# Performance work log

Hardware: AMD Instinct MI355X
Metric: run time of the kernel (lower is better)

The kernel has to match this reference:

```python
import jax, jax.numpy as jnp
import numpy as np
import math

D_MODEL = 1024
NUM_HEADS = 16
D_HEAD = D_MODEL // NUM_HEADS


def setup_inputs() -> dict:
    key = jax.random.key(0)
    ks = jax.random.split(key, 12)
    b, s = 2, 2048
    lim = 1.0 / math.sqrt(D_MODEL)
    def lin_w(k):
        return jax.random.uniform(k, (D_MODEL, D_MODEL), jnp.float32, -lim, lim)
    def lin_b(k):
        return jax.random.uniform(k, (D_MODEL,), jnp.float32, -lim, lim)
    return {
        "q": jax.random.normal(ks[0], (b, s, D_MODEL), jnp.float32),
        "k": jax.random.normal(ks[1], (b, s, D_MODEL), jnp.float32),
        "v": jax.random.normal(ks[2], (b, s, D_MODEL), jnp.float32),
        "mask": jax.random.randint(ks[3], (b, s, s), 0, 2, jnp.int32),
        "Wq": lin_w(ks[4]), "bq": lin_b(ks[5]),
        "Wk": lin_w(ks[6]), "bk": lin_b(ks[7]),
        "Wv": lin_w(ks[8]), "bv": lin_b(ks[9]),
        "Wo": lin_w(ks[10]), "bo": lin_b(ks[11]),
    }


def reference(q, k, v, mask, Wq, bq, Wk, bk, Wv, bv, Wo, bo):
    b, s, _ = q.shape
    h, dh = NUM_HEADS, D_HEAD
    # projections (torch Linear: x @ W.T + b), split heads -> (b, h, s, dh)
    qh = (q @ Wq.T + bq).reshape(b, s, h, dh).transpose(0, 2, 1, 3)
    kh = (k @ Wk.T + bk).reshape(b, s, h, dh).transpose(0, 2, 1, 3)
    vh = (v @ Wv.T + bv).reshape(b, s, h, dh).transpose(0, 2, 1, 3)
    # scaled dot-product scores (b, h, s_q, s_kv)
    scores = jnp.einsum("bhqd,bhkd->bhqk", qh, kh) / math.sqrt(dh)
    scores = jnp.where(mask[:, None, :, :] == 0, jnp.float32(-1e9), scores)
    score = jax.nn.softmax(scores, axis=-1)
    attn = jnp.einsum("bhqk,bhkd->bhqd", score, vh)  # (b, h, s, dh)
    # faithful to the torch code: raw reshape of (b, h, s, dh) -> (b, s, d_model)
    # WITHOUT transposing heads back (replicates the original's .view)
    out = attn.reshape(b, -1, D_MODEL) @ Wo.T + bo
    return out, score
```

## Files before the change

kernel.cpp:

```cpp
#include <hip/hip_runtime.h>

typedef __bf16 bf16_t;
typedef __bf16 bf16x4 __attribute__((ext_vector_type(4)));
typedef __bf16 bf16x8 __attribute__((ext_vector_type(8)));
typedef float f32x4 __attribute__((ext_vector_type(4)));

__device__ __forceinline__ void load_lds16(const void* g, void* l) {
    __builtin_amdgcn_global_load_lds((const __attribute__((address_space(1))) void*)g,
                                     (__attribute__((address_space(3))) void*)l, 16, 0, 0);
}

__global__ void cvt_all_k(const float* __restrict__ q, const float* __restrict__ k,
                          const float* __restrict__ v, const float* __restrict__ wq,
                          const float* __restrict__ wk, const float* __restrict__ wv,
                          const float* __restrict__ wo,
                          bf16_t* __restrict__ oq, bf16_t* __restrict__ ok,
                          bf16_t* __restrict__ ov, bf16_t* __restrict__ owq,
                          bf16_t* __restrict__ owk, bf16_t* __restrict__ owv,
                          bf16_t* __restrict__ owo) {
    int y = blockIdx.y;
    int n = (y < 3) ? 4194304 : 1048576;
    int i = (blockIdx.x * 256 + threadIdx.x) * 4;
    if (i >= n) return;
    const float* s;
    bf16_t* d;
    switch (y) {
        case 0: s = q;  d = oq;  break;
        case 1: s = k;  d = ok;  break;
        case 2: s = v;  d = ov;  break;
        case 3: s = wq; d = owq; break;
        case 4: s = wk; d = owk; break;
        case 5: s = wv; d = owv; break;
        default: s = wo; d = owo; break;
    }
    f32x4 t = *reinterpret_cast<const f32x4*>(s + i);
    *reinterpret_cast<bf16x4*>(d + i) = __builtin_convertvector(t, bf16x4);
}

__global__ void pack_mask_k(const int* __restrict__ mask, unsigned long long* __restrict__ bits) {
    int e = blockIdx.x * blockDim.x + threadIdx.x;
    unsigned long long b = __ballot(mask[e] != 0);
    if ((threadIdx.x & 63) == 0) bits[e >> 6] = b;
}

__global__ __launch_bounds__(256, 3) void gemm_qk(
    const bf16_t* __restrict__ qb, const bf16_t* __restrict__ kb,
    const bf16_t* __restrict__ wq, const bf16_t* __restrict__ wk,
    const float* __restrict__ bq, const float* __restrict__ bk,
    bf16_t* __restrict__ Qh, bf16_t* __restrict__ Kh)
{
    const int z = blockIdx.z;
    const bf16_t* A = z ? kb : qb;
    const bf16_t* W = z ? wk : wq;
    const float* bias = z ? bk : bq;
    bf16_t* obf = z ? Kh : Qh;

    __shared__ bf16_t As[128 * 64];
    __shared__ bf16_t Bs[128 * 64];
    const int tid = threadIdx.x;
    const int lane = tid & 63;
    const int wv = tid >> 6;
    const int wr = wv >> 1, wc = wv & 1;
    const int la = lane & 15, lb = lane >> 4;
    const int bRow = blockIdx.x, bCol = blockIdx.y;
    f32x4 acc[4][4] = {};

    for (int k0 = 0; k0 < 1024; k0 += 64) {
        __syncthreads();
        for (int i = 0; i < 4; ++i) {
            int o = i * 4096 + tid * 16;
            int row = o >> 7;
            int cb = (o & 127) ^ ((row & 7) << 4);
            const char* sa = (const char*)A + (((size_t)(bRow * 128 + row)) * 1024 + k0) * 2 + cb;
            load_lds16(sa, (char*)As + i * 4096 + wv * 1024);
            const char* sb = (const char*)W + (((size_t)(bCol * 128 + row)) * 1024 + k0) * 2 + cb;
            load_lds16(sb, (char*)Bs + i * 4096 + wv * 1024);
        }
        __syncthreads();

        bf16x8 af[2][4], bfr[2][4];
        for (int mi = 0; mi < 4; ++mi) {
            int row = wr * 64 + mi * 16 + la;
            const char* base = (const char*)As + row * 128;
            int sw = (row & 7) << 4;
            af[0][mi] = *reinterpret_cast<const bf16x8*>(base + ((lb * 16) ^ sw));
            af[1][mi] = *reinterpret_cast<const bf16x8*>(base + ((64 + lb * 16) ^ sw));
        }
        for (int ni = 0; ni < 4; ++ni) {
            int row = wc * 64 + ni * 16 + la;
            const char* base = (const char*)Bs + row * 128;
            int sw = (row & 7) << 4;
            bfr[0][ni] = *reinterpret_cast<const bf16x8*>(base + ((lb * 16) ^ sw));
            bfr[1][ni] = *reinterpret_cast<const bf16x8*>(base + ((64 + lb * 16) ^ sw));
        }
        for (int kk = 0; kk < 2; ++kk)
            for (int mi = 0; mi < 4; ++mi)
                for (int ni = 0; ni < 4; ++ni)
                    acc[mi][ni] = __builtin_amdgcn_mfma_f32_16x16x32_bf16(
                        bfr[kk][ni], af[kk][mi], acc[mi][ni], 0, 0, 0);
    }

    for (int mi = 0; mi < 4; ++mi) {
        int n = bRow * 128 + wr * 64 + mi * 16 + la;
        int b_ = n >> 11, s_ = n & 2047;
        for (int ni = 0; ni < 4; ++ni) {
            int colo0 = bCol * 128 + wc * 64 + ni * 16 + lb * 4;
            f32x4 bv4 = *reinterpret_cast<const f32x4*>(&bias[colo0]);
            f32x4 vv = acc[mi][ni] + bv4;
            int h = colo0 >> 6, d0 = colo0 & 63;
            bf16x4 v4 = __builtin_convertvector(vv, bf16x4);
            *reinterpret_cast<bf16x4*>(
                &obf[(((size_t)(b_ * 16 + h) * 2048 + s_) << 6) + d0]) = v4;
        }
    }
}

__global__ __launch_bounds__(256, 3) void gemm_v(
    const bf16_t* __restrict__ vb, const bf16_t* __restrict__ wv_,
    const float* __restrict__ bv, bf16_t* __restrict__ Vt)
{
    __shared__ bf16_t As[128 * 64];
    __shared__ bf16_t Bs[128 * 64];
    const int tid = threadIdx.x;
    const int lane = tid & 63;
    const int wv = tid >> 6;
    const int wr = wv >> 1, wc = wv & 1;
    const int la = lane & 15, lb = lane >> 4;
    const int bRow = blockIdx.x, bCol = blockIdx.y;
    f32x4 acc[4][4] = {};

    for (int k0 = 0; k0 < 1024; k0 += 64) {
        __syncthreads();
        for (int i = 0; i < 4; ++i) {
            int o = i * 4096 + tid * 16;
            int row = o >> 7;
            int cb = (o & 127) ^ ((row & 7) << 4);
            const char* sa = (const char*)vb + (((size_t)(bRow * 128 + row)) * 1024 + k0) * 2 + cb;
            load_lds16(sa, (char*)As + i * 4096 + wv * 1024);
            const char* sb = (const char*)wv_ + (((size_t)(bCol * 128 + row)) * 1024 + k0) * 2 + cb;
            load_lds16(sb, (char*)Bs + i * 4096 + wv * 1024);
        }
        __syncthreads();

        bf16x8 af[2][4], bfr[2][4];
        for (int mi = 0; mi < 4; ++mi) {
            int row = wr * 64 + mi * 16 + la;
            const char* base = (const char*)As + row * 128;
            int sw = (row & 7) << 4;
            af[0][mi] = *reinterpret_cast<const bf16x8*>(base + ((lb * 16) ^ sw));
            af[1][mi] = *reinterpret_cast<const bf16x8*>(base + ((64 + lb * 16) ^ sw));
        }
        for (int ni = 0; ni < 4; ++ni) {
            int row = wc * 64 + ni * 16 + la;
            const char* base = (const char*)Bs + row * 128;
            int sw = (row & 7) << 4;
            bfr[0][ni] = *reinterpret_cast<const bf16x8*>(base + ((lb * 16) ^ sw));
            bfr[1][ni] = *reinterpret_cast<const bf16x8*>(base + ((64 + lb * 16) ^ sw));
        }
        for (int kk = 0; kk < 2; ++kk)
            for (int mi = 0; mi < 4; ++mi)
                for (int ni = 0; ni < 4; ++ni)
                    acc[mi][ni] = __builtin_amdgcn_mfma_f32_16x16x32_bf16(
                        af[kk][mi], bfr[kk][ni], acc[mi][ni], 0, 0, 0);
    }

    for (int ni = 0; ni < 4; ++ni) {
        int colo = bCol * 128 + wc * 64 + ni * 16 + la;
        float bvv = bv[colo];
        int h = colo >> 6, d = colo & 63;
        for (int mi = 0; mi < 4; ++mi) {
            int n0 = bRow * 128 + wr * 64 + mi * 16 + lb * 4;
            int b_ = n0 >> 11, s0 = n0 & 2047;
            f32x4 vv = acc[mi][ni];
            vv[0] += bvv; vv[1] += bvv; vv[2] += bvv; vv[3] += bvv;
            bf16x4 v4 = __builtin_convertvector(vv, bf16x4);
            *reinterpret_cast<bf16x4*>(
                &Vt[((size_t)(b_ * 16 + h) * 64 + d) * 2048 + s0]) = v4;
        }
    }
}

__global__ __launch_bounds__(256, 3) void gemm_out(
    const bf16_t* __restrict__ A, const bf16_t* __restrict__ W,
    const float* __restrict__ bias, float* __restrict__ ofp)
{
    __shared__ bf16_t As[128 * 64];
    __shared__ bf16_t Bs[128 * 64];
    const int tid = threadIdx.x;
    const int lane = tid & 63;
    const int wv = tid >> 6;
    const int wr = wv >> 1, wc = wv & 1;
    const int la = lane & 15, lb = lane >> 4;
    const int bRow = blockIdx.x, bCol = blockIdx.y;
    f32x4 acc[4][4] = {};

    for (int k0 = 0; k0 < 1024; k0 += 64) {
        __syncthreads();
        for (int i = 0; i < 4; ++i) {
            int o = i * 4096 + tid * 16;
            int row = o >> 7;
            int cb = (o & 127) ^ ((row & 7) << 4);
            const char* sa = (const char*)A + (((size_t)(bRow * 128 + row)) * 1024 + k0) * 2 + cb;
            load_lds16(sa, (char*)As + i * 4096 + wv * 1024);
            const char* sb = (const char*)W + (((size_t)(bCol * 128 + row)) * 1024 + k0) * 2 + cb;
            load_lds16(sb, (char*)Bs + i * 4096 + wv * 1024);
        }
        __syncthreads();

        bf16x8 af[2][4], bfr[2][4];
        for (int mi = 0; mi < 4; ++mi) {
            int row = wr * 64 + mi * 16 + la;
            const char* base = (const char*)As + row * 128;
            int sw = (row & 7) << 4;
            af[0][mi] = *reinterpret_cast<const bf16x8*>(base + ((lb * 16) ^ sw));
            af[1][mi] = *reinterpret_cast<const bf16x8*>(base + ((64 + lb * 16) ^ sw));
        }
        for (int ni = 0; ni < 4; ++ni) {
            int row = wc * 64 + ni * 16 + la;
            const char* base = (const char*)Bs + row * 128;
            int sw = (row & 7) << 4;
            bfr[0][ni] = *reinterpret_cast<const bf16x8*>(base + ((lb * 16) ^ sw));
            bfr[1][ni] = *reinterpret_cast<const bf16x8*>(base + ((64 + lb * 16) ^ sw));
        }
        for (int kk = 0; kk < 2; ++kk)
            for (int mi = 0; mi < 4; ++mi)
                for (int ni = 0; ni < 4; ++ni)
                    acc[mi][ni] = __builtin_amdgcn_mfma_f32_16x16x32_bf16(
                        bfr[kk][ni], af[kk][mi], acc[mi][ni], 0, 0, 0);
    }

    for (int mi = 0; mi < 4; ++mi) {
        int n = bRow * 128 + wr * 64 + mi * 16 + la;
        for (int ni = 0; ni < 4; ++ni) {
            int colo0 = bCol * 128 + wc * 64 + ni * 16 + lb * 4;
            f32x4 bv4 = *reinterpret_cast<const f32x4*>(&bias[colo0]);
            f32x4 vv = acc[mi][ni] + bv4;
            __builtin_nontemporal_store(
                vv, reinterpret_cast<f32x4*>(&ofp[(size_t)n * 1024 + colo0]));
        }
    }
}

__global__ __launch_bounds__(512, 4) void attn_fused_k(
    const bf16_t* __restrict__ Qh, const bf16_t* __restrict__ Kh,
    const bf16_t* __restrict__ Vt, const unsigned int* __restrict__ mbits,
    float* __restrict__ P, bf16_t* __restrict__ attn)
{
    __shared__ bf16_t Ks[2][128 * 64];
    __shared__ bf16_t Pb[8][16 * 128];

    const int wg = blockIdx.x;
    const int swg = (wg & 7) * 64 + (wg >> 3);
    const int bh = swg >> 4, qs = swg & 15;

    const int tid = threadIdx.x, lane = tid & 63, wv = tid >> 6;
    const int la = lane & 15, lg = lane >> 4;
    const int b_ = bh >> 4;
    const int qbase = qs * 128 + wv * 16;
    const int swz = (la & 7) << 4;

    bf16x8 qf0, qf1;
    {
        const bf16_t* qrow = Qh + ((size_t)bh * 2048 + qbase + la) * 64 + lg * 8;
        qf0 = *reinterpret_cast<const bf16x8*>(qrow);
        qf1 = *reinterpret_cast<const bf16x8*>(qrow + 32);
    }
    const char* Khb = (const char*)(Kh + ((size_t)bh << 17));
    const bf16_t* Vtb = Vt + ((size_t)bh << 17);
    const unsigned int* mrow = mbits + ((size_t)b_ * 2048 + qbase + la) * 64;
    const float SC = 0.125f * 1.4426950408889634f;

#define STAGE_K(c, bsel)                                                      \
    for (int i = 0; i < 2; ++i) {                                             \
        int o = i * 8192 + tid * 16;                                          \
        int row = o >> 7;                                                     \
        int cb = (o & 127) ^ ((row & 7) << 4);                                \
        load_lds16(Khb + (size_t)(c) * 16384 + row * 128 + cb,                \
                   (char*)Ks[bsel] + i * 8192 + wv * 1024);                   \
    }

    float ssum = 0.f;
    uint4 mws = *reinterpret_cast<const uint4*>(mrow);
    STAGE_K(0, 0)
    __syncthreads();
    for (int c = 0; c < 16; ++c) {
        int cn = (c < 15) ? c + 1 : 15;
        uint4 mnext = *reinterpret_cast<const uint4*>(mrow + cn * 4);
        if (c < 15) { STAGE_K(c + 1, (c + 1) & 1) }
        __builtin_amdgcn_sched_barrier(0);
        const char* Kbase = (const char*)Ks[c & 1];
        unsigned mwarr[4] = {mws.x, mws.y, mws.z, mws.w};
        __builtin_amdgcn_s_setprio(1);
#pragma unroll
        for (int ct = 0; ct < 8; ++ct) {
            int krow = ct * 16 + la;
            const char* kb = Kbase + krow * 128;
            int sw = (krow & 7) << 4;
            bf16x8 kf0 = *reinterpret_cast<const bf16x8*>(kb + ((lg * 16) ^ sw));
            bf16x8 kf1 = *reinterpret_cast<const bf16x8*>(kb + ((64 + lg * 16) ^ sw));
            f32x4 acc = {};
            acc = __builtin_amdgcn_mfma_f32_16x16x32_bf16(kf0, qf0, acc, 0, 0, 0);
            acc = __builtin_amdgcn_mfma_f32_16x16x32_bf16(kf1, qf1, acc, 0, 0, 0);
            unsigned mw = mwarr[ct >> 1];
            int shift = ((ct & 1) << 4) + lg * 4;
            for (int r = 0; r < 4; ++r) {
                float t = __builtin_amdgcn_exp2f(acc[r] * SC);
                ssum += ((mw >> (shift + r)) & 1u) ? t : 0.f;
            }
        }
        __builtin_amdgcn_s_setprio(0);
        __syncthreads();
        mws = mnext;
    }
    ssum += __shfl_xor(ssum, 16, 64);
    ssum += __shfl_xor(ssum, 32, 64);
    const float nls = -__builtin_amdgcn_logf(ssum);

    f32x4 accpv[4] = {};
    float* Pq = P + ((size_t)bh << 22) + (size_t)(qbase + la) * 2048;
    char* Pw = (char*)Pb[wv];
    mws = *reinterpret_cast<const uint4*>(mrow);
    STAGE_K(0, 0)
    __syncthreads();
    for (int c = 0; c < 16; ++c) {
        int cn = (c < 15) ? c + 1 : 15;
        uint4 mnext = *reinterpret_cast<const uint4*>(mrow + cn * 4);
        if (c < 15) { STAGE_K(c + 1, (c + 1) & 1) }
        __builtin_amdgcn_sched_barrier(0);
        const char* Kbase = (const char*)Ks[c & 1];
        unsigned mwarr[4] = {mws.x, mws.y, mws.z, mws.w};
        f32x4 pvbuf[8];
        __builtin_amdgcn_s_setprio(1);
#pragma unroll
        for (int ct = 0; ct < 8; ++ct) {
            int krow = ct * 16 + la;
            const char* kb = Kbase + krow * 128;
            int sw = (krow & 7) << 4;
            bf16x8 kf0 = *reinterpret_cast<const bf16x8*>(kb + ((lg * 16) ^ sw));
            bf16x8 kf1 = *reinterpret_cast<const bf16x8*>(kb + ((64 + lg * 16) ^ sw));
            f32x4 acc = {};
            acc = __builtin_amdgcn_mfma_f32_16x16x32_bf16(kf0, qf0, acc, 0, 0, 0);
            acc = __builtin_amdgcn_mfma_f32_16x16x32_bf16(kf1, qf1, acc, 0, 0, 0);
            unsigned mw = mwarr[ct >> 1];
            int shift = ((ct & 1) << 4) + lg * 4;
            f32x4 pv;
            for (int r = 0; r < 4; ++r) {
                float t = __builtin_amdgcn_exp2f(__builtin_fmaf(acc[r], SC, nls));
                pv[r] = ((mw >> (shift + r)) & 1u) ? t : 0.f;
            }
            pvbuf[ct] = pv;
            bf16x4 pb4 = __builtin_convertvector(pv, bf16x4);
            *reinterpret_cast<bf16x4*>(Pw + ((la * 256 + ct * 32 + lg * 8) ^ swz)) = pb4;
        }
#pragma unroll
        for (int ct = 0; ct < 8; ++ct)
            __builtin_nontemporal_store(
                pvbuf[ct], reinterpret_cast<f32x4*>(Pq + c * 128 + ct * 16 + lg * 4));
        asm volatile("s_waitcnt lgkmcnt(0)" ::: "memory");
        __builtin_amdgcn_sched_barrier(0);
        for (int kbk = 0; kbk < 4; ++kbk) {
            bf16x8 pa = *reinterpret_cast<const bf16x8*>(
                Pw + ((la * 256 + kbk * 64 + lg * 16) ^ swz));
            const bf16_t* vb2 = Vtb + c * 128 + kbk * 32 + lg * 8;
            for (int ni = 0; ni < 4; ++ni) {
                bf16x8 vf = *reinterpret_cast<const bf16x8*>(vb2 + (size_t)(ni * 16 + la) * 2048);
                accpv[ni] = __builtin_amdgcn_mfma_f32_16x16x32_bf16(pa, vf, accpv[ni], 0, 0, 0);
            }
        }
        __builtin_amdgcn_s_setprio(0);
        asm volatile("s_waitcnt vmcnt(8)" ::: "memory");
        __builtin_amdgcn_s_barrier();
        mws = mnext;
    }
#undef STAGE_K

    bf16_t* ab = attn + ((size_t)bh << 17);
    for (int ni = 0; ni < 4; ++ni)
        for (int r = 0; r < 4; ++r)
            ab[(size_t)(qbase + lg * 4 + r) * 64 + ni * 16 + la] = (bf16_t)accpv[ni][r];
}

extern "C" void kernel_launch(void* const* d_in, const int* in_sizes, int n_in,
                              void* d_out, int out_size, void* d_ws, size_t ws_size,
                              hipStream_t stream) {
    const float* q  = (const float*)d_in[0];
    const float* k  = (const float*)d_in[1];
    const float* v  = (const float*)d_in[2];
    const int* mask = (const int*)d_in[3];
    const float* Wq = (const float*)d_in[4];
    const float* bq = (const float*)d_in[5];
    const float* Wk = (const float*)d_in[6];
    const float* bk = (const float*)d_in[7];
    const float* Wv = (const float*)d_in[8];
    const float* bv = (const float*)d_in[9];
    const float* Wo = (const float*)d_in[10];
    const float* bo = (const float*)d_in[11];

    char* ws = (char*)d_ws;
    bf16_t* qb    = (bf16_t*)(ws + 0);
    bf16_t* kb    = (bf16_t*)(ws + 8388608);
    bf16_t* vb    = (bf16_t*)(ws + 16777216);
    bf16_t* wqb   = (bf16_t*)(ws + 25165824);
    bf16_t* wkb   = (bf16_t*)(ws + 27262976);
    bf16_t* wvb   = (bf16_t*)(ws + 29360128);
    bf16_t* wob   = (bf16_t*)(ws + 31457280);
    bf16_t* Qh    = (bf16_t*)(ws + 33554432);
    bf16_t* Kh    = (bf16_t*)(ws + 41943040);
    bf16_t* Vt    = (bf16_t*)(ws + 50331648);
    bf16_t* attnb = (bf16_t*)(ws + 58720256);
    unsigned long long* mbits = (unsigned long long*)(ws + 67108864);

    float* out   = (float*)d_out;
    float* score = out + 4194304;

    cvt_all_k<<<dim3(4096, 7), 256, 0, stream>>>(q, k, v, Wq, Wk, Wv, Wo,
                                                 qb, kb, vb, wqb, wkb, wvb, wob);
    pack_mask_k<<<32768, 256, 0, stream>>>(mask, mbits);

    gemm_qk<<<dim3(32, 8, 2), 256, 0, stream>>>(qb, kb, wqb, wkb, bq, bk, Qh, Kh);
    gemm_v<<<dim3(32, 8), 256, 0, stream>>>(vb, wvb, bv, Vt);

    attn_fused_k<<<512, 512, 0, stream>>>(Qh, Kh, Vt, (const unsigned int*)mbits,
                                          score, attnb);

    gemm_out<<<dim3(32, 8), 256, 0, stream>>>(attnb, wob, bo, out);
}
```

Before: 298.4 us.

## Keep softmax probabilities in registers for PV MFMA via permuted K row mapping

```diff
diff --git a/kernel.cpp b/kernel.cpp
--- a/kernel.cpp
+++ b/kernel.cpp
@@ -4,6 +4,7 @@
 typedef __bf16 bf16x4 __attribute__((ext_vector_type(4)));
 typedef __bf16 bf16x8 __attribute__((ext_vector_type(8)));
 typedef float f32x4 __attribute__((ext_vector_type(4)));
+typedef float f32x8 __attribute__((ext_vector_type(8)));
 
 __device__ __forceinline__ void load_lds16(const void* g, void* l) {
     __builtin_amdgcn_global_load_lds((const __attribute__((address_space(1))) void*)g,
@@ -241,23 +242,21 @@
     }
 }
 
-__global__ __launch_bounds__(512, 4) void attn_fused_k(
+__global__ __launch_bounds__(256, 4) void attn_fused_k(
     const bf16_t* __restrict__ Qh, const bf16_t* __restrict__ Kh,
     const bf16_t* __restrict__ Vt, const unsigned int* __restrict__ mbits,
     float* __restrict__ P, bf16_t* __restrict__ attn)
 {
     __shared__ bf16_t Ks[2][128 * 64];
-    __shared__ bf16_t Pb[8][16 * 128];
 
     const int wg = blockIdx.x;
-    const int swg = (wg & 7) * 64 + (wg >> 3);
-    const int bh = swg >> 4, qs = swg & 15;
+    const int swg = (wg & 7) * 128 + (wg >> 3);
+    const int bh = swg >> 5, qs = swg & 31;
 
     const int tid = threadIdx.x, lane = tid & 63, wv = tid >> 6;
     const int la = lane & 15, lg = lane >> 4;
     const int b_ = bh >> 4;
-    const int qbase = qs * 128 + wv * 16;
-    const int swz = (la & 7) << 4;
+    const int qbase = qs * 64 + wv * 16;
 
     bf16x8 qf0, qf1;
     {
@@ -269,14 +268,16 @@
     const bf16_t* Vtb = Vt + ((size_t)bh << 17);
     const unsigned int* mrow = mbits + ((size_t)b_ * 2048 + qbase + la) * 64;
     const float SC = 0.125f * 1.4426950408889634f;
+    const int krbase = ((la >> 2) << 3) + (la & 3);
+    const int ksw = (((la & 3) | (((la >> 2) & 1) << 2)) << 4);
 
 #define STAGE_K(c, bsel)                                                      \
-    for (int i = 0; i < 2; ++i) {                                             \
-        int o = i * 8192 + tid * 16;                                          \
+    for (int i = 0; i < 4; ++i) {                                             \
+        int o = i * 4096 + tid * 16;                                          \
         int row = o >> 7;                                                     \
-        int cb = (o & 127) ^ ((row & 7) << 4);                                \
+        int cb = (o & 127) ^ ((((row & 3) | (((row >> 3) & 1) << 2))) << 4);  \
         load_lds16(Khb + (size_t)(c) * 16384 + row * 128 + cb,                \
-                   (char*)Ks[bsel] + i * 8192 + wv * 1024);                   \
+                   (char*)Ks[bsel] + i * 4096 + (tid >> 3) * 128);            \
     }
 
     float ssum = 0.f;
@@ -292,20 +293,22 @@
         unsigned mwarr[4] = {mws.x, mws.y, mws.z, mws.w};
         __builtin_amdgcn_s_setprio(1);
 #pragma unroll
-        for (int ct = 0; ct < 8; ++ct) {
-            int krow = ct * 16 + la;
-            const char* kb = Kbase + krow * 128;
-            int sw = (krow & 7) << 4;
-            bf16x8 kf0 = *reinterpret_cast<const bf16x8*>(kb + ((lg * 16) ^ sw));
-            bf16x8 kf1 = *reinterpret_cast<const bf16x8*>(kb + ((64 + lg * 16) ^ sw));
-            f32x4 acc = {};
-            acc = __builtin_amdgcn_mfma_f32_16x16x32_bf16(kf0, qf0, acc, 0, 0, 0);
-            acc = __builtin_amdgcn_mfma_f32_16x16x32_bf16(kf1, qf1, acc, 0, 0, 0);
-            unsigned mw = mwarr[ct >> 1];
-            int shift = ((ct & 1) << 4) + lg * 4;
-            for (int r = 0; r < 4; ++r) {
-                float t = __builtin_amdgcn_exp2f(acc[r] * SC);
-                ssum += ((mw >> (shift + r)) & 1u) ? t : 0.f;
+        for (int t = 0; t < 4; ++t) {
+#pragma unroll
+            for (int h = 0; h < 2; ++h) {
+                int krow = t * 32 + h * 4 + krbase;
+                const char* kb = Kbase + krow * 128;
+                bf16x8 kf0 = *reinterpret_cast<const bf16x8*>(kb + ((lg * 16) ^ ksw));
+                bf16x8 kf1 = *reinterpret_cast<const bf16x8*>(kb + ((64 + lg * 16) ^ ksw));
+                f32x4 acc = {};
+                acc = __builtin_amdgcn_mfma_f32_16x16x32_bf16(kf0, qf0, acc, 0, 0, 0);
+                acc = __builtin_amdgcn_mfma_f32_16x16x32_bf16(kf1, qf1, acc, 0, 0, 0);
+                unsigned mw = mwarr[t];
+                int sh = lg * 8 + h * 4;
+                for (int r = 0; r < 4; ++r) {
+                    float tt = __builtin_amdgcn_exp2f(acc[r] * SC);
+                    ssum += ((mw >> (sh + r)) & 1u) ? tt : 0.f;
+                }
             }
         }
         __builtin_amdgcn_s_setprio(0);
@@ -318,7 +321,6 @@
 
     f32x4 accpv[4] = {};
     float* Pq = P + ((size_t)bh << 22) + (size_t)(qbase + la) * 2048;
-    char* Pw = (char*)Pb[wv];
     mws = *reinterpret_cast<const uint4*>(mrow);
     STAGE_K(0, 0)
     __syncthreads();
@@ -329,39 +331,34 @@
         __builtin_amdgcn_sched_barrier(0);
         const char* Kbase = (const char*)Ks[c & 1];
         unsigned mwarr[4] = {mws.x, mws.y, mws.z, mws.w};
-        f32x4 pvbuf[8];
         __builtin_amdgcn_s_setprio(1);
 #pragma unroll
-        for (int ct = 0; ct < 8; ++ct) {
-            int krow = ct * 16 + la;
-            const char* kb = Kbase + krow * 128;
-            int sw = (krow & 7) << 4;
-            bf16x8 kf0 = *reinterpret_cast<const bf16x8*>(kb + ((lg * 16) ^ sw));
-            bf16x8 kf1 = *reinterpret_cast<const bf16x8*>(kb + ((64 + lg * 16) ^ sw));
-            f32x4 acc = {};
-            acc = __builtin_amdgcn_mfma_f32_16x16x32_bf16(kf0, qf0, acc, 0, 0, 0);
-            acc = __builtin_amdgcn_mfma_f32_16x16x32_bf16(kf1, qf1, acc, 0, 0, 0);
-            unsigned mw = mwarr[ct >> 1];
-            int shift = ((ct & 1) << 4) + lg * 4;
-            f32x4 pv;
-            for (int r = 0; r < 4; ++r) {
-                float t = __builtin_amdgcn_exp2f(__builtin_fmaf(acc[r], SC, nls));
-                pv[r] = ((mw >> (shift + r)) & 1u) ? t : 0.f;
+        for (int t = 0; t < 4; ++t) {
+            f32x4 pv2[2];
+#pragma unroll
+            for (int h = 0; h < 2; ++h) {
+                int krow = t * 32 + h * 4 + krbase;
+                const char* kb = Kbase + krow * 128;
+                bf16x8 kf0 = *reinterpret_cast<const bf16x8*>(kb + ((lg * 16) ^ ksw));
+                bf16x8 kf1 = *reinterpret_cast<const bf16x8*>(kb + ((64 + lg * 16) ^ ksw));
+                f32x4 acc = {};
+                acc = __builtin_amdgcn_mfma_f32_16x16x32_bf16(kf0, qf0, acc, 0, 0, 0);
+                acc = __builtin_amdgcn_mfma_f32_16x16x32_bf16(kf1, qf1, acc, 0, 0, 0);
+                unsigned mw = mwarr[t];
+                int sh = lg * 8 + h * 4;
+                f32x4 pv;
+                for (int r = 0; r < 4; ++r) {
+                    float tt = __builtin_amdgcn_exp2f(__builtin_fmaf(acc[r], SC, nls));
+                    pv[r] = ((mw >> (sh + r)) & 1u) ? tt : 0.f;
+                }
+                pv2[h] = pv;
+                __builtin_nontemporal_store(
+                    pv, reinterpret_cast<f32x4*>(Pq + c * 128 + t * 32 + lg * 8 + h * 4));
             }
-            pvbuf[ct] = pv;
-            bf16x4 pb4 = __builtin_convertvector(pv, bf16x4);
-            *reinterpret_cast<bf16x4*>(Pw + ((la * 256 + ct * 32 + lg * 8) ^ swz)) = pb4;
-        }
-#pragma unroll
-        for (int ct = 0; ct < 8; ++ct)
-            __builtin_nontemporal_store(
-                pvbuf[ct], reinterpret_cast<f32x4*>(Pq + c * 128 + ct * 16 + lg * 4));
-        asm volatile("s_waitcnt lgkmcnt(0)" ::: "memory");
-        __builtin_amdgcn_sched_barrier(0);
-        for (int kbk = 0; kbk < 4; ++kbk) {
-            bf16x8 pa = *reinterpret_cast<const bf16x8*>(
-                Pw + ((la * 256 + kbk * 64 + lg * 16) ^ swz));
-            const bf16_t* vb2 = Vtb + c * 128 + kbk * 32 + lg * 8;
+            f32x8 af8 = {pv2[0][0], pv2[0][1], pv2[0][2], pv2[0][3],
+                         pv2[1][0], pv2[1][1], pv2[1][2], pv2[1][3]};
+            bf16x8 pa = __builtin_convertvector(af8, bf16x8);
+            const bf16_t* vb2 = Vtb + c * 128 + t * 32 + lg * 8;
             for (int ni = 0; ni < 4; ++ni) {
                 bf16x8 vf = *reinterpret_cast<const bf16x8*>(vb2 + (size_t)(ni * 16 + la) * 2048);
                 accpv[ni] = __builtin_amdgcn_mfma_f32_16x16x32_bf16(pa, vf, accpv[ni], 0, 0, 0);
@@ -420,8 +417,8 @@
     gemm_qk<<<dim3(32, 8, 2), 256, 0, stream>>>(qb, kb, wqb, wkb, bq, bk, Qh, Kh);
     gemm_v<<<dim3(32, 8), 256, 0, stream>>>(vb, wvb, bv, Vt);
 
-    attn_fused_k<<<512, 512, 0, stream>>>(Qh, Kh, Vt, (const unsigned int*)mbits,
-                                          score, attnb);
+    attn_fused_k<<<1024, 256, 0, stream>>>(Qh, Kh, Vt, (const unsigned int*)mbits,
+                                           score, attnb);
 
     gemm_out<<<dim3(32, 8), 256, 0, stream>>>(attnb, wob, bo, out);
 }
```

Result: slower. 445.4 us (+49.3%).

## Halve attention tile size and stage V through LDS with deeper K prefetch

Applied to the files above, without the earlier changes.

```diff
diff --git a/kernel.cpp b/kernel.cpp
--- a/kernel.cpp
+++ b/kernel.cpp
@@ -241,22 +241,23 @@
     }
 }
 
-__global__ __launch_bounds__(512, 4) void attn_fused_k(
+__global__ __launch_bounds__(256, 4) void attn_fused_k(
     const bf16_t* __restrict__ Qh, const bf16_t* __restrict__ Kh,
     const bf16_t* __restrict__ Vt, const unsigned int* __restrict__ mbits,
     float* __restrict__ P, bf16_t* __restrict__ attn)
 {
-    __shared__ bf16_t Ks[2][128 * 64];
-    __shared__ bf16_t Pb[8][16 * 128];
+    __shared__ bf16_t Ks[2][64 * 64];
+    __shared__ bf16_t Vs[2][64 * 64];
+    __shared__ bf16_t Pb[4][16 * 64];
 
     const int wg = blockIdx.x;
-    const int swg = (wg & 7) * 64 + (wg >> 3);
-    const int bh = swg >> 4, qs = swg & 15;
+    const int swg = (wg & 7) * 128 + (wg >> 3);
+    const int bh = swg >> 5, qs = swg & 31;
 
     const int tid = threadIdx.x, lane = tid & 63, wv = tid >> 6;
     const int la = lane & 15, lg = lane >> 4;
     const int b_ = bh >> 4;
-    const int qbase = qs * 128 + wv * 16;
+    const int qbase = qs * 64 + wv * 16;
     const int swz = (la & 7) << 4;
 
     bf16x8 qf0, qf1;
@@ -266,41 +267,58 @@
         qf1 = *reinterpret_cast<const bf16x8*>(qrow + 32);
     }
     const char* Khb = (const char*)(Kh + ((size_t)bh << 17));
-    const bf16_t* Vtb = Vt + ((size_t)bh << 17);
+    const char* Vtb = (const char*)(Vt + ((size_t)bh << 17));
     const unsigned int* mrow = mbits + ((size_t)b_ * 2048 + qbase + la) * 64;
     const float SC = 0.125f * 1.4426950408889634f;
 
-#define STAGE_K(c, bsel)                                                      \
+#define STAGE_KD(c, dst)                                                      \
     for (int i = 0; i < 2; ++i) {                                             \
-        int o = i * 8192 + tid * 16;                                          \
+        int o = i * 4096 + tid * 16;                                          \
         int row = o >> 7;                                                     \
         int cb = (o & 127) ^ ((row & 7) << 4);                                \
-        load_lds16(Khb + (size_t)(c) * 16384 + row * 128 + cb,                \
-                   (char*)Ks[bsel] + i * 8192 + wv * 1024);                   \
+        load_lds16(Khb + (size_t)(c) * 8192 + row * 128 + cb, (char*)(dst) + o); \
+    }
+#define STAGE_V(c, bsel)                                                      \
+    for (int i = 0; i < 2; ++i) {                                             \
+        int o = i * 4096 + tid * 16;                                          \
+        int row = o >> 7;                                                     \
+        int cb = (o & 127) ^ ((row & 7) << 4);                                \
+        load_lds16(Vtb + (size_t)row * 4096 + (size_t)(c) * 128 + cb,         \
+                   (char*)Vs[bsel] + o);                                      \
+    }
+
+#define QK_TILE(ct, Kbase, acc)                                               \
+    {                                                                         \
+        int krow = (ct) * 16 + la;                                            \
+        const char* kb = (Kbase) + krow * 128;                                \
+        int sw = (krow & 7) << 4;                                             \
+        bf16x8 kf0 = *reinterpret_cast<const bf16x8*>(kb + ((lg * 16) ^ sw)); \
+        bf16x8 kf1 = *reinterpret_cast<const bf16x8*>(kb + ((64 + lg * 16) ^ sw)); \
+        acc = __builtin_amdgcn_mfma_f32_16x16x32_bf16(kf0, qf0, acc, 0, 0, 0); \
+        acc = __builtin_amdgcn_mfma_f32_16x16x32_bf16(kf1, qf1, acc, 0, 0, 0); \
     }
 
     float ssum = 0.f;
-    uint4 mws = *reinterpret_cast<const uint4*>(mrow);
-    STAGE_K(0, 0)
-    __syncthreads();
-    for (int c = 0; c < 16; ++c) {
-        int cn = (c < 15) ? c + 1 : 15;
-        uint4 mnext = *reinterpret_cast<const uint4*>(mrow + cn * 4);
-        if (c < 15) { STAGE_K(c + 1, (c + 1) & 1) }
+    uint2 mws = *reinterpret_cast<const uint2*>(mrow);
+    STAGE_KD(0, Ks[0])
+    STAGE_KD(1, Ks[1])
+    asm volatile("s_waitcnt vmcnt(2)" ::: "memory");
+    __builtin_amdgcn_s_barrier();
+    for (int c = 0; c < 32; ++c) {
+        uint2 mnext = *reinterpret_cast<const uint2*>(mrow + 2 * ((c + 1) & 31));
+        {
+            int cs = (c + 2) & 31;
+            char* dst = ((c + 2) & 2) ? (char*)Vs[(c + 2) & 1] : (char*)Ks[(c + 2) & 1];
+            STAGE_KD(cs, dst)
+        }
         __builtin_amdgcn_sched_barrier(0);
-        const char* Kbase = (const char*)Ks[c & 1];
-        unsigned mwarr[4] = {mws.x, mws.y, mws.z, mws.w};
+        const char* Kbase = (c & 2) ? (const char*)Vs[c & 1] : (const char*)Ks[c & 1];
+        unsigned mwarr[2] = {mws.x, mws.y};
         __builtin_amdgcn_s_setprio(1);
 #pragma unroll
-        for (int ct = 0; ct < 8; ++ct) {
-            int krow = ct * 16 + la;
-            const char* kb = Kbase + krow * 128;
-            int sw = (krow & 7) << 4;
-            bf16x8 kf0 = *reinterpret_cast<const bf16x8*>(kb + ((lg * 16) ^ sw));
-            bf16x8 kf1 = *reinterpret_cast<const bf16x8*>(kb + ((64 + lg * 16) ^ sw));
+        for (int ct = 0; ct < 4; ++ct) {
             f32x4 acc = {};
-            acc = __builtin_amdgcn_mfma_f32_16x16x32_bf16(kf0, qf0, acc, 0, 0, 0);
-            acc = __builtin_amdgcn_mfma_f32_16x16x32_bf16(kf1, qf1, acc, 0, 0, 0);
+            QK_TILE(ct, Kbase, acc)
             unsigned mw = mwarr[ct >> 1];
             int shift = ((ct & 1) << 4) + lg * 4;
             for (int r = 0; r < 4; ++r) {
@@ -309,9 +327,11 @@
             }
         }
         __builtin_amdgcn_s_setprio(0);
-        __syncthreads();
+        asm volatile("s_waitcnt vmcnt(3)" ::: "memory");
+        __builtin_amdgcn_s_barrier();
         mws = mnext;
     }
+    asm volatile("s_waitcnt vmcnt(0)" ::: "memory");
     ssum += __shfl_xor(ssum, 16, 64);
     ssum += __shfl_xor(ssum, 32, 64);
     const float nls = -__builtin_amdgcn_logf(ssum);
@@ -319,28 +339,25 @@
     f32x4 accpv[4] = {};
     float* Pq = P + ((size_t)bh << 22) + (size_t)(qbase + la) * 2048;
     char* Pw = (char*)Pb[wv];
-    mws = *reinterpret_cast<const uint4*>(mrow);
-    STAGE_K(0, 0)
-    __syncthreads();
-    for (int c = 0; c < 16; ++c) {
-        int cn = (c < 15) ? c + 1 : 15;
-        uint4 mnext = *reinterpret_cast<const uint4*>(mrow + cn * 4);
-        if (c < 15) { STAGE_K(c + 1, (c + 1) & 1) }
+    mws = *reinterpret_cast<const uint2*>(mrow);
+    STAGE_V(0, 0)
+    asm volatile("s_waitcnt vmcnt(0)" ::: "memory");
+    __builtin_amdgcn_s_barrier();
+    for (int c = 0; c < 32; ++c) {
+        int cn = (c + 1) & 31;
+        uint2 mnext = *reinterpret_cast<const uint2*>(mrow + 2 * cn);
+        STAGE_KD(cn, Ks[cn & 1])
+        STAGE_V(cn, cn & 1)
         __builtin_amdgcn_sched_barrier(0);
         const char* Kbase = (const char*)Ks[c & 1];
-        unsigned mwarr[4] = {mws.x, mws.y, mws.z, mws.w};
-        f32x4 pvbuf[8];
+        const char* Vbase = (const char*)Vs[c & 1];
+        unsigned mwarr[2] = {mws.x, mws.y};
+        f32x4 pvbuf[4];
         __builtin_amdgcn_s_setprio(1);
 #pragma unroll
-        for (int ct = 0; ct < 8; ++ct) {
-            int krow = ct * 16 + la;
-            const char* kb = Kbase + krow * 128;
-            int sw = (krow & 7) << 4;
-            bf16x8 kf0 = *reinterpret_cast<const bf16x8*>(kb + ((lg * 16) ^ sw));
-            bf16x8 kf1 = *reinterpret_cast<const bf16x8*>(kb + ((64 + lg * 16) ^ sw));
+        for (int ct = 0; ct < 4; ++ct) {
             f32x4 acc = {};
-            acc = __builtin_amdgcn_mfma_f32_16x16x32_bf16(kf0, qf0, acc, 0, 0, 0);
-            acc = __builtin_amdgcn_mfma_f32_16x16x32_bf16(kf1, qf1, acc, 0, 0, 0);
+            QK_TILE(ct, Kbase, acc)
             unsigned mw = mwarr[ct >> 1];
             int shift = ((ct & 1) << 4) + lg * 4;
             f32x4 pv;
@@ -350,29 +367,33 @@
             }
             pvbuf[ct] = pv;
             bf16x4 pb4 = __builtin_convertvector(pv, bf16x4);
-            *reinterpret_cast<bf16x4*>(Pw + ((la * 256 + ct * 32 + lg * 8) ^ swz)) = pb4;
+            *reinterpret_cast<bf16x4*>(Pw + ((la * 128 + ct * 32 + lg * 8) ^ swz)) = pb4;
         }
 #pragma unroll
-        for (int ct = 0; ct < 8; ++ct)
+        for (int ct = 0; ct < 4; ++ct)
             __builtin_nontemporal_store(
-                pvbuf[ct], reinterpret_cast<f32x4*>(Pq + c * 128 + ct * 16 + lg * 4));
+                pvbuf[ct], reinterpret_cast<f32x4*>(Pq + c * 64 + ct * 16 + lg * 4));
         asm volatile("s_waitcnt lgkmcnt(0)" ::: "memory");
         __builtin_amdgcn_sched_barrier(0);
-        for (int kbk = 0; kbk < 4; ++kbk) {
+#pragma unroll
+        for (int kbk = 0; kbk < 2; ++kbk) {
             bf16x8 pa = *reinterpret_cast<const bf16x8*>(
-                Pw + ((la * 256 + kbk * 64 + lg * 16) ^ swz));
-            const bf16_t* vb2 = Vtb + c * 128 + kbk * 32 + lg * 8;
+                Pw + ((la * 128 + kbk * 64 + lg * 16) ^ swz));
             for (int ni = 0; ni < 4; ++ni) {
-                bf16x8 vf = *reinterpret_cast<const bf16x8*>(vb2 + (size_t)(ni * 16 + la) * 2048);
+                int vrow = ni * 16 + la;
+                bf16x8 vf = *reinterpret_cast<const bf16x8*>(
+                    Vbase + vrow * 128 + ((kbk * 64 + lg * 16) ^ ((vrow & 7) << 4)));
                 accpv[ni] = __builtin_amdgcn_mfma_f32_16x16x32_bf16(pa, vf, accpv[ni], 0, 0, 0);
             }
         }
         __builtin_amdgcn_s_setprio(0);
-        asm volatile("s_waitcnt vmcnt(8)" ::: "memory");
+        asm volatile("s_waitcnt lgkmcnt(0) vmcnt(4)" ::: "memory");
         __builtin_amdgcn_s_barrier();
         mws = mnext;
     }
-#undef STAGE_K
+#undef STAGE_KD
+#undef STAGE_V
+#undef QK_TILE
 
     bf16_t* ab = attn + ((size_t)bh << 17);
     for (int ni = 0; ni < 4; ++ni)
@@ -420,8 +441,8 @@
     gemm_qk<<<dim3(32, 8, 2), 256, 0, stream>>>(qb, kb, wqb, wkb, bq, bk, Qh, Kh);
     gemm_v<<<dim3(32, 8), 256, 0, stream>>>(vb, wvb, bv, Vt);
 
-    attn_fused_k<<<512, 512, 0, stream>>>(Qh, Kh, Vt, (const unsigned int*)mbits,
-                                          score, attnb);
+    attn_fused_k<<<1024, 256, 0, stream>>>(Qh, Kh, Vt, (const unsigned int*)mbits,
+                                           score, attnb);
 
     gemm_out<<<dim3(32, 8), 256, 0, stream>>>(attnb, wob, bo, out);
 }
```

New measurement: 299.1 us. Within noise of the previous version (+0.2%).
